# Kernel tuning notes

Hardware: AMD Instinct MI355X
Metric: run time of the kernel (lower is better)

Reference implementation:

```python
import jax, jax.numpy as jnp
import numpy as np
from jax import lax

B, H, W, C = 16, 32, 32, 256
HEADS = 8
HD = C // HEADS          # attention_head_dim = 32
KSZ = 3                  # conv_kernel_size
DIL = 2                  # dilation_rate
SCALE = HD ** -0.5


def setup_inputs() -> dict:
    key = jax.random.key(0)
    k0, k1, k2, k3 = jax.random.split(key, 4)
    return {
        "query": jax.random.normal(k0, (B, H, W, C), jnp.float32),
        "key_in": jax.random.normal(k1, (B, H, W, C), jnp.float32),
        "value": jax.random.normal(k2, (B, H, W, C), jnp.float32),
        # depthwise conv: kernel [kh, kw, in_ch/groups=1, out_ch=C], plus bias [C]
        "conv_kernel": jax.random.normal(k3, (KSZ, KSZ, 1, C), jnp.float32) * 0.05,
        "conv_bias": jnp.zeros((C,), jnp.float32),
    }


def _dwconv(x, kernel, bias):
    # depthwise dilated conv, padding SAME (Keras Conv2D groups=C)
    y = lax.conv_general_dilated(
        x, kernel,
        window_strides=(1, 1), padding="SAME",
        rhs_dilation=(DIL, DIL),
        dimension_numbers=("NHWC", "HWIO", "NHWC"),
        feature_group_count=C,
    )
    return y + bias


def _to_heads(x):
    # [B,H,W,C] -> [B, heads, S, head_dim]
    return x.reshape(B, H * W, HEADS, HD).transpose(0, 2, 1, 3)


def reference(query, key_in, value, conv_kernel, conv_bias):
    q = _to_heads(query)
    k = _to_heads(_dwconv(key_in, conv_kernel, conv_bias))
    v = _to_heads(_dwconv(value, conv_kernel, conv_bias))
    scores = jnp.einsum("bhqd,bhkd->bhqk", q, k) * SCALE  # [B,heads,S,S]
    attn = jax.nn.softmax(scores, axis=-1)
    out = jnp.einsum("bhqk,bhkd->bhqd", attn, v)          # [B,heads,S,hd]
    return out.transpose(0, 2, 1, 3).reshape(B, H, W, C)
```

## Files before the change

### kernel.cpp

```cpp
#include <hip/hip_runtime.h>

#define B_    16
#define HH    32
#define WW    32
#define CC    256
#define HEADS 8
#define HD    32
#define S_    1024
#define KT    128
#define NITER (S_ / KT)
#define SCALE_L2E 0.25503486f

typedef unsigned short u16;
typedef unsigned int   u32;
typedef __attribute__((ext_vector_type(8))) short short8;
typedef __attribute__((ext_vector_type(4))) float f32x4;

__device__ __forceinline__ u16 f2bf(float f) {
    u32 x = __float_as_uint(f);
    return (u16)((x + 0x7fffu + ((x >> 16) & 1u)) >> 16);
}

__global__ __launch_bounds__(256) void dw_conv_kernel(
    const float* __restrict__ key_in, const float* __restrict__ value,
    const float* __restrict__ ck, const float* __restrict__ cb,
    u16* __restrict__ Kws, u16* __restrict__ Vws)
{
    int idx = blockIdx.x * 256 + threadIdx.x;
    int c = idx & 255;
    int x = (idx >> 8) & 31;
    int y = (idx >> 13) & 31;
    int b = idx >> 18;

    float bias = cb[c];
    float ka = bias, va = bias;
    #pragma unroll
    for (int kh = 0; kh < 3; kh++) {
        int yy = y + kh * 2 - 2;
        if (yy < 0 || yy >= HH) continue;
        #pragma unroll
        for (int kw = 0; kw < 3; kw++) {
            int xx = x + kw * 2 - 2;
            if (xx < 0 || xx >= WW) continue;
            float w = ck[(kh * 3 + kw) * CC + c];
            size_t ii = ((((size_t)b * HH + yy) * WW) + xx) * CC + c;
            ka += w * key_in[ii];
            va += w * value[ii];
        }
    }
    int h = c >> 5, d = c & 31;
    int s = y * WW + x;
    size_t o = (((size_t)(b * HEADS + h)) * S_ + s) * HD + d;
    Kws[o] = f2bf(ka * SCALE_L2E);
    Vws[o] = f2bf(va);
}

__global__ __launch_bounds__(256) void attn_kernel(
    const float* __restrict__ query,
    const u16* __restrict__ Kws, const u16* __restrict__ Vws,
    float* __restrict__ out)
{
    __shared__ __align__(16) u16 Klds[KT][40];
    __shared__ __align__(16) u16 Vtlds[HD][KT + 8];

    const int tid  = threadIdx.x;
    const int lane = tid & 63;
    const int wv   = tid >> 6;
    const int q15  = lane & 15;
    const int quad = lane >> 4;

    const int blk = blockIdx.x;
    const int bh  = blk >> 3;
    const int qt  = blk & 7;
    const int b = bh >> 3, h = bh & 7;
    const int q0w = qt * 128 + wv * 32;

    short8 qf[2];
    #pragma unroll
    for (int f = 0; f < 2; f++) {
        const float* qp = query + ((size_t)(b * S_ + q0w + f * 16 + q15)) * CC
                          + h * HD + quad * 8;
        float4 a = *(const float4*)(qp);
        float4 c = *(const float4*)(qp + 4);
        short8 v;
        v[0] = (short)f2bf(a.x); v[1] = (short)f2bf(a.y);
        v[2] = (short)f2bf(a.z); v[3] = (short)f2bf(a.w);
        v[4] = (short)f2bf(c.x); v[5] = (short)f2bf(c.y);
        v[6] = (short)f2bf(c.z); v[7] = (short)f2bf(c.w);
        qf[f] = v;
    }

    short8 ones;
    #pragma unroll
    for (int j = 0; j < 8; j++) ones[j] = (short)0x3F80;

    const u16* Kg = Kws + (size_t)bh * S_ * HD;
    const u16* Vg = Vws + (size_t)bh * S_ * HD;

    f32x4 Ot[2][2];
    f32x4 Dsum[2];
    #pragma unroll
    for (int f = 0; f < 2; f++) {
        Ot[f][0] = (f32x4)0.f; Ot[f][1] = (f32x4)0.f; Dsum[f] = (f32x4)0.f;
    }

    for (int it = 0; it < NITER; it++) {
        const int kt0 = it * KT;
        __syncthreads();

        {
            int row = tid >> 1, half = tid & 1;
            const uint4* src = (const uint4*)(Kg + (size_t)(kt0 + row) * HD + half * 16);
            uint4 s0 = src[0], s1 = src[1];
            uint4* dst = (uint4*)&Klds[row][half * 16];
            dst[0] = s0; dst[1] = s1;
        }
        {
            int g  = tid >> 3;
            int s4 = tid & 7;
            int c = g >> 3, w = g & 7, t2 = (w >> 2) & 1, qd = w & 3;
            int pg = (c << 5) | (qd << 3) | (t2 << 2);
            const uint2* vsrc = (const uint2*)(Vg + (size_t)(kt0 + 4 * g) * HD + 4 * s4);
            uint2 r0 = vsrc[0], r1 = vsrc[8], r2 = vsrc[16], r3 = vsrc[24];
            u32 p01, p23;
            p01 = __builtin_amdgcn_perm(r1.x, r0.x, 0x05040100u);
            p23 = __builtin_amdgcn_perm(r3.x, r2.x, 0x05040100u);
            *(uint2*)&Vtlds[4 * s4 + 0][pg] = make_uint2(p01, p23);
            p01 = __builtin_amdgcn_perm(r1.x, r0.x, 0x07060302u);
            p23 = __builtin_amdgcn_perm(r3.x, r2.x, 0x07060302u);
            *(uint2*)&Vtlds[4 * s4 + 1][pg] = make_uint2(p01, p23);
            p01 = __builtin_amdgcn_perm(r1.y, r0.y, 0x05040100u);
            p23 = __builtin_amdgcn_perm(r3.y, r2.y, 0x05040100u);
            *(uint2*)&Vtlds[4 * s4 + 2][pg] = make_uint2(p01, p23);
            p01 = __builtin_amdgcn_perm(r1.y, r0.y, 0x07060302u);
            p23 = __builtin_amdgcn_perm(r3.y, r2.y, 0x07060302u);
            *(uint2*)&Vtlds[4 * s4 + 3][pg] = make_uint2(p01, p23);
        }
        __syncthreads();

        f32x4 St[2][8];
        #pragma unroll
        for (int t = 0; t < 8; t++) {
            short8 kf = *(const short8*)&Klds[t * 16 + q15][quad * 8];
            St[0][t] = __builtin_amdgcn_mfma_f32_16x16x32_bf16(kf, qf[0], (f32x4)0.f, 0, 0, 0);
            St[1][t] = __builtin_amdgcn_mfma_f32_16x16x32_bf16(kf, qf[1], (f32x4)0.f, 0, 0, 0);
        }

        #pragma unroll
        for (int f = 0; f < 2; f++)
            #pragma unroll
            for (int t = 0; t < 8; t++)
                #pragma unroll
                for (int r = 0; r < 4; r++)
                    St[f][t][r] = __builtin_amdgcn_exp2f(St[f][t][r]);

        #pragma unroll
        for (int c = 0; c < 4; c++) {
            short8 vf0 = *(const short8*)&Vtlds[q15][c * 32 + quad * 8];
            short8 vf1 = *(const short8*)&Vtlds[16 + q15][c * 32 + quad * 8];
            #pragma unroll
            for (int f = 0; f < 2; f++) {
                union { u32 u[4]; short8 s8; } pk;
                pk.u[0] = __builtin_amdgcn_perm(__float_as_uint(St[f][2*c][1]),
                                                __float_as_uint(St[f][2*c][0]), 0x07060302u);
                pk.u[1] = __builtin_amdgcn_perm(__float_as_uint(St[f][2*c][3]),
                                                __float_as_uint(St[f][2*c][2]), 0x07060302u);
                pk.u[2] = __builtin_amdgcn_perm(__float_as_uint(St[f][2*c+1][1]),
                                                __float_as_uint(St[f][2*c+1][0]), 0x07060302u);
                pk.u[3] = __builtin_amdgcn_perm(__float_as_uint(St[f][2*c+1][3]),
                                                __float_as_uint(St[f][2*c+1][2]), 0x07060302u);
                Ot[f][0] = __builtin_amdgcn_mfma_f32_16x16x32_bf16(vf0, pk.s8, Ot[f][0], 0, 0, 0);
                Ot[f][1] = __builtin_amdgcn_mfma_f32_16x16x32_bf16(vf1, pk.s8, Ot[f][1], 0, 0, 0);
                Dsum[f]  = __builtin_amdgcn_mfma_f32_16x16x32_bf16(ones, pk.s8, Dsum[f], 0, 0, 0);
            }
        }
    }

    #pragma unroll
    for (int f = 0; f < 2; f++) {
        float inv = 1.0f / Dsum[f][0];
        int qg = q0w + f * 16 + q15;
        float* op = out + ((size_t)(b * S_ + qg)) * CC + h * HD;
        #pragma unroll
        for (int h2 = 0; h2 < 2; h2++)
            #pragma unroll
            for (int r = 0; r < 4; r++)
                op[h2 * 16 + quad * 4 + r] = Ot[f][h2][r] * inv;
    }
}

extern "C" void kernel_launch(void* const* d_in, const int* in_sizes, int n_in,
                              void* d_out, int out_size, void* d_ws, size_t ws_size,
                              hipStream_t stream)
{
    const float* query  = (const float*)d_in[0];
    const float* key_in = (const float*)d_in[1];
    const float* value  = (const float*)d_in[2];
    const float* ck     = (const float*)d_in[3];
    const float* cb     = (const float*)d_in[4];
    float* out = (float*)d_out;

    u16* Kws = (u16*)d_ws;
    u16* Vws = Kws + (size_t)B_ * HEADS * S_ * HD;

    dw_conv_kernel<<<(B_ * HH * WW * CC) / 256, 256, 0, stream>>>(
        key_in, value, ck, cb, Kws, Vws);

    attn_kernel<<<(B_ * HEADS * S_) / 128, 256, 0, stream>>>(
        query, Kws, Vws, out);
}
```

Baseline: 149.3 us.

## Double-buffer K/V tiles in LDS and interleave QK with PV per chunk

The attention kernel now keeps two LDS buffers for K and transposed V. It issues the global loads for the next tile into registers before computing on the current one and writes them to the other buffer afterwards, so there is one barrier per iteration instead of two. The QK MFMAs, exp2 and PV MFMAs are interleaved per 32-key chunk rather than computing all scores first, which cuts live registers. Launch bounds now request 4 blocks per CU. The cost is doubled LDS use and extra registers to hold the prefetched data.

```diff
diff --git a/kernel.cpp b/kernel.cpp
--- a/kernel.cpp
+++ b/kernel.cpp
@@ -55,13 +55,13 @@
     Vws[o] = f2bf(va);
 }
 
-__global__ __launch_bounds__(256) void attn_kernel(
+__global__ __launch_bounds__(256, 4) void attn_kernel(
     const float* __restrict__ query,
     const u16* __restrict__ Kws, const u16* __restrict__ Vws,
     float* __restrict__ out)
 {
-    __shared__ __align__(16) u16 Klds[KT][40];
-    __shared__ __align__(16) u16 Vtlds[HD][KT + 8];
+    __shared__ __align__(16) u16 Klds[2][KT][40];
+    __shared__ __align__(16) u16 Vtlds[2][HD][KT + 8];
 
     const int tid  = threadIdx.x;
     const int lane = tid & 63;
@@ -97,6 +97,39 @@
     const u16* Kg = Kws + (size_t)bh * S_ * HD;
     const u16* Vg = Vws + (size_t)bh * S_ * HD;
 
+    const int krow = tid >> 1, khalf = tid & 1;
+    const int vg  = tid >> 3, vs4 = tid & 7;
+    const int vc = vg >> 3, vw = vg & 7;
+    const int vt2 = (vw >> 2) & 1, vqd = vw & 3;
+    const int vpg = (vc << 5) | (vqd << 3) | (vt2 << 2);
+
+    uint4 kra, krb;
+    uint2 vr0, vr1, vr2, vr3;
+
+    auto issue_loads = [&](int kt0) {
+        const uint4* ksrc = (const uint4*)(Kg + (size_t)(kt0 + krow) * HD + khalf * 16);
+        kra = ksrc[0]; krb = ksrc[1];
+        const uint2* vsrc = (const uint2*)(Vg + (size_t)(kt0 + 4 * vg) * HD + 4 * vs4);
+        vr0 = vsrc[0]; vr1 = vsrc[8]; vr2 = vsrc[16]; vr3 = vsrc[24];
+    };
+    auto write_lds = [&](int p) {
+        uint4* kdst = (uint4*)&Klds[p][krow][khalf * 16];
+        kdst[0] = kra; kdst[1] = krb;
+        u32 a, bb;
+        a  = __builtin_amdgcn_perm(vr1.x, vr0.x, 0x05040100u);
+        bb = __builtin_amdgcn_perm(vr3.x, vr2.x, 0x05040100u);
+        *(uint2*)&Vtlds[p][4 * vs4 + 0][vpg] = make_uint2(a, bb);
+        a  = __builtin_amdgcn_perm(vr1.x, vr0.x, 0x07060302u);
+        bb = __builtin_amdgcn_perm(vr3.x, vr2.x, 0x07060302u);
+        *(uint2*)&Vtlds[p][4 * vs4 + 1][vpg] = make_uint2(a, bb);
+        a  = __builtin_amdgcn_perm(vr1.y, vr0.y, 0x05040100u);
+        bb = __builtin_amdgcn_perm(vr3.y, vr2.y, 0x05040100u);
+        *(uint2*)&Vtlds[p][4 * vs4 + 2][vpg] = make_uint2(a, bb);
+        a  = __builtin_amdgcn_perm(vr1.y, vr0.y, 0x07060302u);
+        bb = __builtin_amdgcn_perm(vr3.y, vr2.y, 0x07060302u);
+        *(uint2*)&Vtlds[p][4 * vs4 + 3][vpg] = make_uint2(a, bb);
+    };
+
     f32x4 Ot[2][2];
     f32x4 Dsum[2];
     #pragma unroll
@@ -104,76 +137,44 @@
         Ot[f][0] = (f32x4)0.f; Ot[f][1] = (f32x4)0.f; Dsum[f] = (f32x4)0.f;
     }
 
+    issue_loads(0);
+    write_lds(0);
+
     for (int it = 0; it < NITER; it++) {
-        const int kt0 = it * KT;
+        const int p = it & 1;
+        if (it + 1 < NITER) issue_loads((it + 1) * KT);
         __syncthreads();
-
-        {
-            int row = tid >> 1, half = tid & 1;
-            const uint4* src = (const uint4*)(Kg + (size_t)(kt0 + row) * HD + half * 16);
-            uint4 s0 = src[0], s1 = src[1];
-            uint4* dst = (uint4*)&Klds[row][half * 16];
-            dst[0] = s0; dst[1] = s1;
-        }
-        {
-            int g  = tid >> 3;
-            int s4 = tid & 7;
-            int c = g >> 3, w = g & 7, t2 = (w >> 2) & 1, qd = w & 3;
-            int pg = (c << 5) | (qd << 3) | (t2 << 2);
-            const uint2* vsrc = (const uint2*)(Vg + (size_t)(kt0 + 4 * g) * HD + 4 * s4);
-            uint2 r0 = vsrc[0], r1 = vsrc[8], r2 = vsrc[16], r3 = vsrc[24];
-            u32 p01, p23;
-            p01 = __builtin_amdgcn_perm(r1.x, r0.x, 0x05040100u);
-            p23 = __builtin_amdgcn_perm(r3.x, r2.x, 0x05040100u);
-            *(uint2*)&Vtlds[4 * s4 + 0][pg] = make_uint2(p01, p23);
-            p01 = __builtin_amdgcn_perm(r1.x, r0.x, 0x07060302u);
-            p23 = __builtin_amdgcn_perm(r3.x, r2.x, 0x07060302u);
-            *(uint2*)&Vtlds[4 * s4 + 1][pg] = make_uint2(p01, p23);
-            p01 = __builtin_amdgcn_perm(r1.y, r0.y, 0x05040100u);
-            p23 = __builtin_amdgcn_perm(r3.y, r2.y, 0x05040100u);
-            *(uint2*)&Vtlds[4 * s4 + 2][pg] = make_uint2(p01, p23);
-            p01 = __builtin_amdgcn_perm(r1.y, r0.y, 0x07060302u);
-            p23 = __builtin_amdgcn_perm(r3.y, r2.y, 0x07060302u);
-            *(uint2*)&Vtlds[4 * s4 + 3][pg] = make_uint2(p01, p23);
-        }
-        __syncthreads();
-
-        f32x4 St[2][8];
-        #pragma unroll
-        for (int t = 0; t < 8; t++) {
-            short8 kf = *(const short8*)&Klds[t * 16 + q15][quad * 8];
-            St[0][t] = __builtin_amdgcn_mfma_f32_16x16x32_bf16(kf, qf[0], (f32x4)0.f, 0, 0, 0);
-            St[1][t] = __builtin_amdgcn_mfma_f32_16x16x32_bf16(kf, qf[1], (f32x4)0.f, 0, 0, 0);
-        }
-
-        #pragma unroll
-        for (int f = 0; f < 2; f++)
-            #pragma unroll
-            for (int t = 0; t < 8; t++)
-                #pragma unroll
-                for (int r = 0; r < 4; r++)
-                    St[f][t][r] = __builtin_amdgcn_exp2f(St[f][t][r]);
 
         #pragma unroll
         for (int c = 0; c < 4; c++) {
-            short8 vf0 = *(const short8*)&Vtlds[q15][c * 32 + quad * 8];
-            short8 vf1 = *(const short8*)&Vtlds[16 + q15][c * 32 + quad * 8];
+            short8 kf0 = *(const short8*)&Klds[p][c * 32 + q15][quad * 8];
+            short8 kf1 = *(const short8*)&Klds[p][c * 32 + 16 + q15][quad * 8];
+            short8 vf0 = *(const short8*)&Vtlds[p][q15][c * 32 + quad * 8];
+            short8 vf1 = *(const short8*)&Vtlds[p][16 + q15][c * 32 + quad * 8];
             #pragma unroll
             for (int f = 0; f < 2; f++) {
+                f32x4 s0 = __builtin_amdgcn_mfma_f32_16x16x32_bf16(kf0, qf[f], (f32x4)0.f, 0, 0, 0);
+                f32x4 s1 = __builtin_amdgcn_mfma_f32_16x16x32_bf16(kf1, qf[f], (f32x4)0.f, 0, 0, 0);
+                #pragma unroll
+                for (int r = 0; r < 4; r++) {
+                    s0[r] = __builtin_amdgcn_exp2f(s0[r]);
+                    s1[r] = __builtin_amdgcn_exp2f(s1[r]);
+                }
                 union { u32 u[4]; short8 s8; } pk;
-                pk.u[0] = __builtin_amdgcn_perm(__float_as_uint(St[f][2*c][1]),
-                                                __float_as_uint(St[f][2*c][0]), 0x07060302u);
-                pk.u[1] = __builtin_amdgcn_perm(__float_as_uint(St[f][2*c][3]),
-                                                __float_as_uint(St[f][2*c][2]), 0x07060302u);
-                pk.u[2] = __builtin_amdgcn_perm(__float_as_uint(St[f][2*c+1][1]),
-                                                __float_as_uint(St[f][2*c+1][0]), 0x07060302u);
-                pk.u[3] = __builtin_amdgcn_perm(__float_as_uint(St[f][2*c+1][3]),
-                                                __float_as_uint(St[f][2*c+1][2]), 0x07060302u);
+                pk.u[0] = __builtin_amdgcn_perm(__float_as_uint(s0[1]),
+                                                __float_as_uint(s0[0]), 0x07060302u);
+                pk.u[1] = __builtin_amdgcn_perm(__float_as_uint(s0[3]),
+                                                __float_as_uint(s0[2]), 0x07060302u);
+                pk.u[2] = __builtin_amdgcn_perm(__float_as_uint(s1[1]),
+                                                __float_as_uint(s1[0]), 0x07060302u);
+                pk.u[3] = __builtin_amdgcn_perm(__float_as_uint(s1[3]),
+                                                __float_as_uint(s1[2]), 0x07060302u);
                 Ot[f][0] = __builtin_amdgcn_mfma_f32_16x16x32_bf16(vf0, pk.s8, Ot[f][0], 0, 0, 0);
                 Ot[f][1] = __builtin_amdgcn_mfma_f32_16x16x32_bf16(vf1, pk.s8, Ot[f][1], 0, 0, 0);
                 Dsum[f]  = __builtin_amdgcn_mfma_f32_16x16x32_bf16(ones, pk.s8, Dsum[f], 0, 0, 0);
             }
         }
+        if (it + 1 < NITER) write_lds((it + 1) & 1);
     }
 
     #pragma unroll
```

Result: faster. 144.7 us (-3.1%).
